# Kernel tuning notes

Hardware: AMD Instinct MI355X
Metric: run time of the kernel (lower is better)

## Reference

```python
import jax, jax.numpy as jnp
import numpy as np

C = 256
C8 = C // 8


def setup_inputs() -> dict:
    key = jax.random.key(0)
    ks = jax.random.split(key, 9)
    B, H, W = 4, 64, 64
    s = 1.0 / np.sqrt(C)
    return {
        "pre_feat": jax.random.normal(ks[0], (B, C, H, W), jnp.float32),
        "post_feat": jax.random.normal(ks[1], (B, C, H, W), jnp.float32),
        "Wq": jax.random.normal(ks[2], (C8, C), jnp.float32) * s,
        "bq": jnp.zeros((C8,), jnp.float32),
        "Wk": jax.random.normal(ks[3], (C8, C), jnp.float32) * s,
        "bk": jnp.zeros((C8,), jnp.float32),
        "Wv": jax.random.normal(ks[4], (C, C), jnp.float32) * s,
        "bv": jnp.zeros((C,), jnp.float32),
        "gamma": jnp.zeros((1,), jnp.float32),
    }


def reference(pre_feat, post_feat, Wq, bq, Wk, bk, Wv, bv, gamma):
    B, Cc, H, W = pre_feat.shape
    N = H * W
    pre = pre_feat.reshape(B, Cc, N)    # (B, C, N)
    post = post_feat.reshape(B, Cc, N)
    # 1x1 convs == per-pixel linear projections
    q = jnp.einsum('dc,bcn->bdn', Wq, post) + bq[None, :, None]  # (B, C8, N)
    k = jnp.einsum('dc,bcn->bdn', Wk, pre) + bk[None, :, None]   # (B, C8, N)
    v = jnp.einsum('dc,bcn->bdn', Wv, pre) + bv[None, :, None]   # (B, C, N)
    # energy[b,i,j] = <q[b,:,i], k[b,:,j]>  (unscaled)
    energy = jnp.einsum('bdi,bdj->bij', q, k)                    # (B, N, N)
    attention = jax.nn.softmax(energy, axis=-1)
    # out[b,c,i] = sum_j v[b,c,j] * attention[b,i,j]
    out = jnp.einsum('bcj,bij->bci', v, attention).reshape(B, Cc, H, W)
    return gamma[0] * out + post_feat
```

## Files before the change

### kernel.cpp

```cpp
#include <hip/hip_runtime.h>

#define Bn 4
#define Cn 256
#define Dn 32
#define Nn 4096

typedef __bf16 bf16x8 __attribute__((ext_vector_type(8)));
typedef short shortx4 __attribute__((ext_vector_type(4)));
typedef float f32x4 __attribute__((ext_vector_type(4)));

__device__ __forceinline__ float bf2f(unsigned short u) {
  unsigned int v = ((unsigned int)u) << 16;
  return __builtin_bit_cast(float, v);
}
__device__ __forceinline__ unsigned short f2bf(float f) {
  unsigned int v = __builtin_bit_cast(unsigned int, f);
  v += 0x7FFFu + ((v >> 16) & 1u);
  return (unsigned short)(v >> 16);
}
__device__ __forceinline__ bf16x8 ldfrag(const unsigned short* p) {
  return __builtin_bit_cast(bf16x8, *(const uint4*)p);
}
__device__ __forceinline__ uint4 pack8(const float* p) {
  float4 a = *(const float4*)p;
  float4 b = *(const float4*)(p + 4);
  union { unsigned short s[8]; uint4 u; } x;
  x.s[0] = f2bf(a.x); x.s[1] = f2bf(a.y); x.s[2] = f2bf(a.z); x.s[3] = f2bf(a.w);
  x.s[4] = f2bf(b.x); x.s[5] = f2bf(b.y); x.s[6] = f2bf(b.z); x.s[7] = f2bf(b.w);
  return x.u;
}
__device__ __forceinline__ uint4 pack4x2(const float* p0, const float* p1) {
  float4 a = *(const float4*)p0;
  float4 b = *(const float4*)p1;
  union { unsigned short s[8]; uint4 u; } x;
  x.s[0] = f2bf(a.x); x.s[1] = f2bf(a.y); x.s[2] = f2bf(a.z); x.s[3] = f2bf(a.w);
  x.s[4] = f2bf(b.x); x.s[5] = f2bf(b.y); x.s[6] = f2bf(b.z); x.s[7] = f2bf(b.w);
  return x.u;
}
__device__ __forceinline__ void async16(unsigned short* lds, const unsigned short* g) {
  __builtin_amdgcn_global_load_lds(
      (const __attribute__((address_space(1))) unsigned int*)g,
      (__attribute__((address_space(3))) unsigned int*)lds, 16, 0, 0);
}

__global__ __launch_bounds__(256) void conv_weights(
    const float* __restrict__ Wq, const float* __restrict__ Wk,
    const float* __restrict__ Wv, unsigned short* __restrict__ WqBf,
    unsigned short* __restrict__ WkBf, unsigned short* __restrict__ WvBf)
{
  int idx8 = (blockIdx.x * 256 + threadIdx.x) * 8;
  if (idx8 < 8192) {
    *(uint4*)(WqBf + idx8) = pack8(Wq + idx8);
  } else if (idx8 < 16384) {
    *(uint4*)(WkBf + idx8 - 8192) = pack8(Wk + idx8 - 8192);
  } else {
    *(uint4*)(WvBf + idx8 - 16384) = pack8(Wv + idx8 - 16384);
  }
}

__global__ __launch_bounds__(256) void qk_proj(
    const float* __restrict__ pre, const float* __restrict__ post,
    const unsigned short* __restrict__ WqBf, const float* __restrict__ bq,
    const unsigned short* __restrict__ WkBf, const float* __restrict__ bk,
    unsigned short* __restrict__ Qt, unsigned short* __restrict__ Kt,
    unsigned short* __restrict__ preBf)
{
  __shared__ __align__(16) unsigned short sPre[64][40];
  __shared__ __align__(16) unsigned short sPost[64][40];
  __shared__ __align__(16) float sRed[4][64][16];

  const int tid = threadIdx.x;
  const int lane = tid & 63, w = tid >> 6;
  const int quad = lane >> 4, n16 = lane & 15;
  const int b = blockIdx.x >> 7;
  const int i0 = (blockIdx.x & 127) << 5;
  const int iSub = w & 1, cHalf = w >> 1;

  const float* preB = pre + (size_t)b * Cn * Nn;
  const float* postB = post + (size_t)b * Cn * Nn;

  const f32x4 zz = {0.f, 0.f, 0.f, 0.f};
  f32x4 accQ[2] = {zz, zz}, accK[2] = {zz, zz};

  const int cc = tid >> 2, q = tid & 3;
  const int gcol = ((n16 >> 2) << 3) + (iSub << 2) + (n16 & 3);

  for (int it = 0; it < 4; it++) {
    const int cs = it * 64;
    const float* pPost = postB + (size_t)(cs + cc) * Nn + i0;
    const float* pPre  = preB  + (size_t)(cs + cc) * Nn + i0;
    uint4 pkPost = pack4x2(pPost + q * 4, pPost + 16 + q * 4);
    uint4 pkPre  = pack4x2(pPre  + q * 4, pPre  + 16 + q * 4);
    __syncthreads();
    *(uint4*)&sPost[cc][q * 8] = pkPost;
    *(uint4*)&sPre[cc][q * 8]  = pkPre;
    *(uint4*)(preBf + ((size_t)b * Cn + cs + cc) * Nn + i0 + q * 8) = pkPre;
    __syncthreads();

    union { unsigned short s[8]; bf16x8 v; } up, ur;
#pragma unroll
    for (int jj = 0; jj < 8; jj++) {
      up.s[jj] = sPost[cHalf * 32 + quad * 8 + jj][gcol];
      ur.s[jj] = sPre[cHalf * 32 + quad * 8 + jj][gcol];
    }
    const int c0g = cs + cHalf * 32 + quad * 8;
#pragma unroll
    for (int dt = 0; dt < 2; dt++) {
      bf16x8 aq = ldfrag(WqBf + (size_t)(dt * 16 + n16) * Cn + c0g);
      accQ[dt] = __builtin_amdgcn_mfma_f32_16x16x32_bf16(aq, up.v, accQ[dt], 0, 0, 0);
      bf16x8 ak = ldfrag(WkBf + (size_t)(dt * 16 + n16) * Cn + c0g);
      accK[dt] = __builtin_amdgcn_mfma_f32_16x16x32_bf16(ak, ur.v, accK[dt], 0, 0, 0);
    }
  }

  __syncthreads();
#pragma unroll
  for (int dt = 0; dt < 2; dt++) {
    *(f32x4*)&sRed[w][lane][dt * 4] = accQ[dt];
    *(f32x4*)&sRed[w][lane][8 + dt * 4] = accK[dt];
  }
  __syncthreads();
  if (w < 2) {
    const int ii = i0 + iSub * 16 + n16;
#pragma unroll
    for (int dt = 0; dt < 2; dt++) {
      f32x4 qv = *(f32x4*)&sRed[w][lane][dt * 4];
      f32x4 q2 = *(f32x4*)&sRed[w + 2][lane][dt * 4];
      f32x4 kv = *(f32x4*)&sRed[w][lane][8 + dt * 4];
      f32x4 k2 = *(f32x4*)&sRed[w + 2][lane][8 + dt * 4];
      union { unsigned short s[4]; uint2 u; } oq, ok;
#pragma unroll
      for (int r = 0; r < 4; r++) {
        int d = dt * 16 + quad * 4 + r;
        oq.s[r] = f2bf(qv[r] + q2[r] + bq[d]);
        ok.s[r] = f2bf(kv[r] + k2[r] + bk[d]);
      }
      *(uint2*)(Qt + ((size_t)b * Nn + ii) * Dn + dt * 16 + quad * 4) = oq.u;
      *(uint2*)(Kt + ((size_t)b * Nn + ii) * Dn + dt * 16 + quad * 4) = ok.u;
    }
  }
}

__global__ __launch_bounds__(128, 2) void flash_attn(
    const unsigned short* __restrict__ Qt, const unsigned short* __restrict__ Kt,
    const unsigned short* __restrict__ preBf,
    unsigned short* __restrict__ Opart, float* __restrict__ Lpart)
{
  __shared__ __align__(16) unsigned short sX[256 * 64];
  __shared__ __align__(16) unsigned short sK[64][40];

  const int tid = threadIdx.x;
  const int lane = tid & 63, w = tid >> 6;
  const int quad = lane >> 4, n16 = lane & 15;
  const int b = blockIdx.x >> 8;
  const int js = (blockIdx.x >> 6) & 3;
  const int it = blockIdx.x & 63;
  const int iw = it * 64 + w * 32;

  bf16x8 qf[2];
#pragma unroll
  for (int sub = 0; sub < 2; sub++)
    qf[sub] = ldfrag(Qt + ((size_t)b * Nn + iw + sub * 16 + n16) * Dn + quad * 8);

  const f32x4 zz = {0.f, 0.f, 0.f, 0.f};
  f32x4 acc[2][16];
#pragma unroll
  for (int sub = 0; sub < 2; sub++)
#pragma unroll
    for (int ct = 0; ct < 16; ct++) acc[sub][ct] = zz;
  float lrow[2] = {0.f, 0.f};

  const int lrw = lane >> 3;
  const size_t laneoff = (size_t)lrw * Nn + (size_t)(((lane & 7) ^ lrw) << 3);
  const unsigned short* preB = preBf + (size_t)b * Cn * Nn + laneoff;
  const int xsw = n16 & 7;
  const int xoff0 = ((quad) ^ xsw) << 3;
  const int xoff1 = ((4 + quad) ^ xsw) << 3;

  for (int j0 = js * 1024; j0 < js * 1024 + 1024; j0 += 64) {
    __syncthreads();
#pragma unroll
    for (int k = 0; k < 2; k++) {
      int s = tid + k * 128;
      int row = s >> 2, seg = (s & 3) << 3;
      *(uint4*)&sK[row][seg] =
          *(const uint4*)(Kt + ((size_t)b * Nn + j0 + row) * Dn + seg);
    }
#pragma unroll
    for (int k = 0; k < 16; k++) {
      const int rb = (k * 2 + w) * 8;
      async16(sX + rb * 64 + (lane << 3), preB + (size_t)rb * Nn + j0);
    }
    __syncthreads();

    f32x4 sc[2][4];
#pragma unroll
    for (int jt = 0; jt < 4; jt++) {
      bf16x8 akf = ldfrag(&sK[jt * 16 + n16][quad * 8]);
      sc[0][jt] = __builtin_amdgcn_mfma_f32_16x16x32_bf16(akf, qf[0], zz, 0, 0, 0);
      sc[1][jt] = __builtin_amdgcn_mfma_f32_16x16x32_bf16(akf, qf[1], zz, 0, 0, 0);
    }

    shortx4 pb[2][4];
#pragma unroll
    for (int sub = 0; sub < 2; sub++) {
      float ps = 0.f;
#pragma unroll
      for (int jt = 0; jt < 4; jt++) {
        union { unsigned short s[4]; shortx4 v; } u;
#pragma unroll
        for (int r = 0; r < 4; r++) {
          float p = __expf(fminf(sc[sub][jt][r], 70.f));
          ps += p;
          u.s[r] = f2bf(p);
        }
        pb[sub][jt] = u.v;
      }
      ps += __shfl_xor(ps, 16);
      ps += __shfl_xor(ps, 32);
      lrow[sub] += ps;
    }

#pragma unroll
    for (int jt2 = 0; jt2 < 2; jt2++) {
      const int xoff = jt2 ? xoff1 : xoff0;
#pragma unroll
      for (int ct = 0; ct < 16; ct++) {
        union { bf16x8 v; shortx4 h[2]; } av;
        av.v = ldfrag(&sX[(ct * 16 + n16) * 64 + xoff]);
        acc[0][ct] = __builtin_amdgcn_mfma_f32_16x16x16bf16_1k(av.h[0], pb[0][jt2 * 2], acc[0][ct], 0, 0, 0);
        acc[0][ct] = __builtin_amdgcn_mfma_f32_16x16x16bf16_1k(av.h[1], pb[0][jt2 * 2 + 1], acc[0][ct], 0, 0, 0);
        acc[1][ct] = __builtin_amdgcn_mfma_f32_16x16x16bf16_1k(av.h[0], pb[1][jt2 * 2], acc[1][ct], 0, 0, 0);
        acc[1][ct] = __builtin_amdgcn_mfma_f32_16x16x16bf16_1k(av.h[1], pb[1][jt2 * 2 + 1], acc[1][ct], 0, 0, 0);
      }
    }
  }

  const size_t base = (size_t)(js * 4 + b) * Nn;
#pragma unroll
  for (int sub = 0; sub < 2; sub++) {
    const int i = iw + sub * 16 + n16;
    if (quad == 0) Lpart[base + i] = lrow[sub];
#pragma unroll
    for (int ct = 0; ct < 16; ct++) {
      union { unsigned short s[4]; uint2 u; } pk;
#pragma unroll
      for (int r = 0; r < 4; r++) pk.s[r] = f2bf(acc[sub][ct][r]);
      *(uint2*)(Opart + (base + i) * 256 + ct * 16 + quad * 4) = pk.u;
    }
  }
}

__global__ __launch_bounds__(256) void combine(
    const unsigned short* __restrict__ Opart, const float* __restrict__ Lpart,
    const unsigned short* __restrict__ WvBf, const float* __restrict__ bv,
    const float* __restrict__ post, const float* __restrict__ gamma,
    float* __restrict__ out)
{
  __shared__ __align__(16) unsigned short sU[64 * 264];
  __shared__ float sL[64];

  const int tid = threadIdx.x;
  const int lane = tid & 63, w = tid >> 6;
  const int quad = lane >> 4, n16 = lane & 15;
  const int b = blockIdx.x >> 6;
  const int i0 = (blockIdx.x & 63) << 6;

  if (tid < 64) {
    float l = 0.f;
#pragma unroll
    for (int js = 0; js < 4; js++) l += Lpart[(size_t)(js * 4 + b) * Nn + i0 + tid];
    sL[tid] = 1.f / l;
  }
  __syncthreads();

#pragma unroll
  for (int pass = 0; pass < 8; pass++) {
    const int il = pass * 8 + (tid >> 5);
    const int c8 = (tid & 31) << 3;
    const float inv = sL[il];
    float a[8] = {0.f, 0.f, 0.f, 0.f, 0.f, 0.f, 0.f, 0.f};
#pragma unroll
    for (int js = 0; js < 4; js++) {
      uint4 u = *(const uint4*)(Opart + ((size_t)(js * 4 + b) * Nn + i0 + il) * 256 + c8);
      const unsigned short* us = (const unsigned short*)&u;
#pragma unroll
      for (int e = 0; e < 8; e++) a[e] += bf2f(us[e]);
    }
    union { unsigned short s[8]; uint4 u; } pk;
#pragma unroll
    for (int e = 0; e < 8; e++) pk.s[e] = f2bf(a[e] * inv);
    *(uint4*)&sU[il * 264 + c8] = pk.u;
  }
  __syncthreads();

  bf16x8 ub[8];
#pragma unroll
  for (int kc = 0; kc < 8; kc++)
    ub[kc] = ldfrag(&sU[(w * 16 + n16) * 264 + kc * 32 + quad * 8]);

  const float g = gamma[0];
  const f32x4 zz = {0.f, 0.f, 0.f, 0.f};
#pragma unroll
  for (int ct2 = 0; ct2 < 16; ct2++) {
    f32x4 o = zz;
#pragma unroll
    for (int kc = 0; kc < 8; kc++) {
      bf16x8 awv = ldfrag(WvBf + (size_t)(ct2 * 16 + n16) * Cn + kc * 32 + quad * 8);
      o = __builtin_amdgcn_mfma_f32_16x16x32_bf16(awv, ub[kc], o, 0, 0, 0);
    }
#pragma unroll
    for (int r = 0; r < 4; r++) {
      const int c = ct2 * 16 + quad * 4 + r;
      const size_t addr = ((size_t)b * Cn + c) * Nn + i0 + w * 16 + n16;
      out[addr] = g * (o[r] + bv[c]) + post[addr];
    }
  }
}

extern "C" void kernel_launch(void* const* d_in, const int* in_sizes, int n_in,
                              void* d_out, int out_size, void* d_ws, size_t ws_size,
                              hipStream_t stream) {
  const float* pre   = (const float*)d_in[0];
  const float* post  = (const float*)d_in[1];
  const float* Wq    = (const float*)d_in[2];
  const float* bq    = (const float*)d_in[3];
  const float* Wk    = (const float*)d_in[4];
  const float* bk    = (const float*)d_in[5];
  const float* Wv    = (const float*)d_in[6];
  const float* bv    = (const float*)d_in[7];
  const float* gamma = (const float*)d_in[8];
  float* out = (float*)d_out;

  char* ws = (char*)d_ws;
  unsigned short* Qt    = (unsigned short*)ws;
  unsigned short* Kt    = Qt + (size_t)Bn * Nn * Dn;
  unsigned short* preBf = Kt + (size_t)Bn * Nn * Dn;
  unsigned short* WqBf  = preBf + (size_t)Bn * Cn * Nn;
  unsigned short* WkBf  = WqBf + Dn * Cn;
  unsigned short* WvBf  = WkBf + Dn * Cn;
  unsigned short* Opart = WvBf + Cn * Cn;
  float* Lpart = (float*)(Opart + (size_t)4 * Bn * Nn * Cn);

  conv_weights<<<40, 256, 0, stream>>>(Wq, Wk, Wv, WqBf, WkBf, WvBf);
  qk_proj<<<512, 256, 0, stream>>>(pre, post, WqBf, bq, WkBf, bk, Qt, Kt, preBf);
  flash_attn<<<1024, 128, 0, stream>>>(Qt, Kt, preBf, Opart, Lpart);
  combine<<<256, 256, 0, stream>>>(Opart, Lpart, WvBf, bv, post, gamma, out);
}
```

Baseline: 215.8 us.

## Restructure prep/projection, pipeline flash attention K/P, and regrid combine

The weight conversion is merged with a new prep kernel that converts pre and post to bf16 and writes pixel-major transposed copies, so qk_proj becomes a plain MFMA loop over contiguous rows. Q is prescaled by log2(e) so the softmax uses exp2f. The flash attention loop now loads K fragments straight from global into registers and computes the next tile's probabilities while the current tile's PV MFMAs run, removing the K shared-memory staging. The combine kernel uses 512 smaller blocks, and packed bf16 conversion intrinsics replace manual rounding. The cost is an extra transposed bf16 copy of the inputs aliased into the Opart workspace, plus more registers in flash_attn.

```diff
diff --git a/kernel.cpp b/kernel.cpp
--- a/kernel.cpp
+++ b/kernel.cpp
@@ -1,4 +1,5 @@
 #include <hip/hip_runtime.h>
+#include <hip/hip_bf16.h>
 
 #define Bn 4
 #define Cn 256
@@ -18,23 +19,20 @@
   v += 0x7FFFu + ((v >> 16) & 1u);
   return (unsigned short)(v >> 16);
 }
+__device__ __forceinline__ unsigned int pk2(float a, float b) {
+  union { __hip_bfloat162 h; unsigned int u; } x;
+  x.h = __float22bfloat162_rn(make_float2(a, b));
+  return x.u;
+}
 __device__ __forceinline__ bf16x8 ldfrag(const unsigned short* p) {
   return __builtin_bit_cast(bf16x8, *(const uint4*)p);
 }
 __device__ __forceinline__ uint4 pack8(const float* p) {
   float4 a = *(const float4*)p;
   float4 b = *(const float4*)(p + 4);
-  union { unsigned short s[8]; uint4 u; } x;
-  x.s[0] = f2bf(a.x); x.s[1] = f2bf(a.y); x.s[2] = f2bf(a.z); x.s[3] = f2bf(a.w);
-  x.s[4] = f2bf(b.x); x.s[5] = f2bf(b.y); x.s[6] = f2bf(b.z); x.s[7] = f2bf(b.w);
-  return x.u;
-}
-__device__ __forceinline__ uint4 pack4x2(const float* p0, const float* p1) {
-  float4 a = *(const float4*)p0;
-  float4 b = *(const float4*)p1;
-  union { unsigned short s[8]; uint4 u; } x;
-  x.s[0] = f2bf(a.x); x.s[1] = f2bf(a.y); x.s[2] = f2bf(a.z); x.s[3] = f2bf(a.w);
-  x.s[4] = f2bf(b.x); x.s[5] = f2bf(b.y); x.s[6] = f2bf(b.z); x.s[7] = f2bf(b.w);
+  union { unsigned int u2[4]; uint4 u; } x;
+  x.u2[0] = pk2(a.x, a.y); x.u2[1] = pk2(a.z, a.w);
+  x.u2[2] = pk2(b.x, b.y); x.u2[3] = pk2(b.z, b.w);
   return x.u;
 }
 __device__ __forceinline__ void async16(unsigned short* lds, const unsigned short* g) {
@@ -43,102 +41,100 @@
       (__attribute__((address_space(3))) unsigned int*)lds, 16, 0, 0);
 }
 
-__global__ __launch_bounds__(256) void conv_weights(
+__global__ __launch_bounds__(256) void prep(
+    const float* __restrict__ pre, const float* __restrict__ post,
     const float* __restrict__ Wq, const float* __restrict__ Wk,
-    const float* __restrict__ Wv, unsigned short* __restrict__ WqBf,
+    const float* __restrict__ Wv,
+    unsigned short* __restrict__ preT, unsigned short* __restrict__ postT,
+    unsigned short* __restrict__ preBf, unsigned short* __restrict__ WqBf,
     unsigned short* __restrict__ WkBf, unsigned short* __restrict__ WvBf)
 {
-  int idx8 = (blockIdx.x * 256 + threadIdx.x) * 8;
-  if (idx8 < 8192) {
-    *(uint4*)(WqBf + idx8) = pack8(Wq + idx8);
-  } else if (idx8 < 16384) {
-    *(uint4*)(WkBf + idx8 - 8192) = pack8(Wk + idx8 - 8192);
-  } else {
-    *(uint4*)(WvBf + idx8 - 16384) = pack8(Wv + idx8 - 16384);
-  }
+  if (blockIdx.x >= 1024) {
+    int idx8 = ((blockIdx.x - 1024) * 256 + threadIdx.x) * 8;
+    if (idx8 < 8192) {
+      *(uint4*)(WqBf + idx8) = pack8(Wq + idx8);
+    } else if (idx8 < 16384) {
+      *(uint4*)(WkBf + idx8 - 8192) = pack8(Wk + idx8 - 8192);
+    } else {
+      *(uint4*)(WvBf + idx8 - 16384) = pack8(Wv + idx8 - 16384);
+    }
+    return;
+  }
+  __shared__ __align__(16) unsigned short sA[64][72];
+  __shared__ __align__(16) unsigned short sB[64][72];
+  const int tid = threadIdx.x;
+  const int b = blockIdx.x >> 8;
+  const int c0 = ((blockIdx.x >> 6) & 3) << 6;
+  const int i0 = (blockIdx.x & 63) << 6;
+  const int r = tid >> 2, ch = (tid & 3) << 4;
+
+  const float* pPost = post + ((size_t)b * Cn + c0 + r) * Nn + i0 + ch;
+  const float* pPre  = pre  + ((size_t)b * Cn + c0 + r) * Nn + i0 + ch;
+  *(uint4*)&sA[r][ch]     = pack8(pPost);
+  *(uint4*)&sA[r][ch + 8] = pack8(pPost + 8);
+  uint4 pb0 = pack8(pPre), pb1 = pack8(pPre + 8);
+  *(uint4*)&sB[r][ch]     = pb0;
+  *(uint4*)&sB[r][ch + 8] = pb1;
+  __syncthreads();
+
+#pragma unroll
+  for (int e = 0; e < 2; e++) {
+    int h = ((tid & 3) << 1) + e;
+    int g = (h >> 2) << 5, q = (h & 3) << 2;
+    union { unsigned short s[8]; uint4 u; } o;
+    *(uint2*)&o.s[0] = *(const uint2*)&sB[r][g + q];
+    *(uint2*)&o.s[4] = *(const uint2*)&sB[r][g + 16 + q];
+    *(uint4*)(preBf + ((size_t)b * Cn + c0 + r) * Nn + i0 + h * 8) = o.u;
+  }
+  union { unsigned short s[16]; uint4 u[2]; } tp, tk;
+#pragma unroll
+  for (int e = 0; e < 16; e++) {
+    tp.s[e] = sA[ch + e][r];
+    tk.s[e] = sB[ch + e][r];
+  }
+  const size_t trow = ((size_t)b * Nn + i0 + r) * Cn + c0 + ch;
+  *(uint4*)(postT + trow) = tp.u[0];
+  *(uint4*)(postT + trow + 8) = tp.u[1];
+  *(uint4*)(preT + trow) = tk.u[0];
+  *(uint4*)(preT + trow + 8) = tk.u[1];
 }
 
 __global__ __launch_bounds__(256) void qk_proj(
-    const float* __restrict__ pre, const float* __restrict__ post,
+    const unsigned short* __restrict__ preT, const unsigned short* __restrict__ postT,
     const unsigned short* __restrict__ WqBf, const float* __restrict__ bq,
     const unsigned short* __restrict__ WkBf, const float* __restrict__ bk,
-    unsigned short* __restrict__ Qt, unsigned short* __restrict__ Kt,
-    unsigned short* __restrict__ preBf)
+    unsigned short* __restrict__ Qt, unsigned short* __restrict__ Kt)
 {
-  __shared__ __align__(16) unsigned short sPre[64][40];
-  __shared__ __align__(16) unsigned short sPost[64][40];
-  __shared__ __align__(16) float sRed[4][64][16];
-
   const int tid = threadIdx.x;
   const int lane = tid & 63, w = tid >> 6;
   const int quad = lane >> 4, n16 = lane & 15;
   const int b = blockIdx.x >> 7;
   const int i0 = (blockIdx.x & 127) << 5;
-  const int iSub = w & 1, cHalf = w >> 1;
-
-  const float* preB = pre + (size_t)b * Cn * Nn;
-  const float* postB = post + (size_t)b * Cn * Nn;
+  const int isub = w & 1, dh = w >> 1;
+  const int i = i0 + isub * 16 + n16;
+  const size_t rowB = ((size_t)b * Nn + i) * Cn;
 
   const f32x4 zz = {0.f, 0.f, 0.f, 0.f};
-  f32x4 accQ[2] = {zz, zz}, accK[2] = {zz, zz};
-
-  const int cc = tid >> 2, q = tid & 3;
-  const int gcol = ((n16 >> 2) << 3) + (iSub << 2) + (n16 & 3);
-
-  for (int it = 0; it < 4; it++) {
-    const int cs = it * 64;
-    const float* pPost = postB + (size_t)(cs + cc) * Nn + i0;
-    const float* pPre  = preB  + (size_t)(cs + cc) * Nn + i0;
-    uint4 pkPost = pack4x2(pPost + q * 4, pPost + 16 + q * 4);
-    uint4 pkPre  = pack4x2(pPre  + q * 4, pPre  + 16 + q * 4);
-    __syncthreads();
-    *(uint4*)&sPost[cc][q * 8] = pkPost;
-    *(uint4*)&sPre[cc][q * 8]  = pkPre;
-    *(uint4*)(preBf + ((size_t)b * Cn + cs + cc) * Nn + i0 + q * 8) = pkPre;
-    __syncthreads();
-
-    union { unsigned short s[8]; bf16x8 v; } up, ur;
-#pragma unroll
-    for (int jj = 0; jj < 8; jj++) {
-      up.s[jj] = sPost[cHalf * 32 + quad * 8 + jj][gcol];
-      ur.s[jj] = sPre[cHalf * 32 + quad * 8 + jj][gcol];
-    }
-    const int c0g = cs + cHalf * 32 + quad * 8;
-#pragma unroll
-    for (int dt = 0; dt < 2; dt++) {
-      bf16x8 aq = ldfrag(WqBf + (size_t)(dt * 16 + n16) * Cn + c0g);
-      accQ[dt] = __builtin_amdgcn_mfma_f32_16x16x32_bf16(aq, up.v, accQ[dt], 0, 0, 0);
-      bf16x8 ak = ldfrag(WkBf + (size_t)(dt * 16 + n16) * Cn + c0g);
-      accK[dt] = __builtin_amdgcn_mfma_f32_16x16x32_bf16(ak, ur.v, accK[dt], 0, 0, 0);
-    }
-  }
-
-  __syncthreads();
-#pragma unroll
-  for (int dt = 0; dt < 2; dt++) {
-    *(f32x4*)&sRed[w][lane][dt * 4] = accQ[dt];
-    *(f32x4*)&sRed[w][lane][8 + dt * 4] = accK[dt];
-  }
-  __syncthreads();
-  if (w < 2) {
-    const int ii = i0 + iSub * 16 + n16;
-#pragma unroll
-    for (int dt = 0; dt < 2; dt++) {
-      f32x4 qv = *(f32x4*)&sRed[w][lane][dt * 4];
-      f32x4 q2 = *(f32x4*)&sRed[w + 2][lane][dt * 4];
-      f32x4 kv = *(f32x4*)&sRed[w][lane][8 + dt * 4];
-      f32x4 k2 = *(f32x4*)&sRed[w + 2][lane][8 + dt * 4];
-      union { unsigned short s[4]; uint2 u; } oq, ok;
-#pragma unroll
-      for (int r = 0; r < 4; r++) {
-        int d = dt * 16 + quad * 4 + r;
-        oq.s[r] = f2bf(qv[r] + q2[r] + bq[d]);
-        ok.s[r] = f2bf(kv[r] + k2[r] + bk[d]);
-      }
-      *(uint2*)(Qt + ((size_t)b * Nn + ii) * Dn + dt * 16 + quad * 4) = oq.u;
-      *(uint2*)(Kt + ((size_t)b * Nn + ii) * Dn + dt * 16 + quad * 4) = ok.u;
-    }
-  }
+  f32x4 aq = zz, ak = zz;
+#pragma unroll
+  for (int kc = 0; kc < 8; kc++) {
+    bf16x8 bfq = ldfrag(postT + rowB + kc * 32 + quad * 8);
+    bf16x8 bfk = ldfrag(preT + rowB + kc * 32 + quad * 8);
+    bf16x8 awq = ldfrag(WqBf + (size_t)(dh * 16 + n16) * Cn + kc * 32 + quad * 8);
+    bf16x8 awk = ldfrag(WkBf + (size_t)(dh * 16 + n16) * Cn + kc * 32 + quad * 8);
+    aq = __builtin_amdgcn_mfma_f32_16x16x32_bf16(awq, bfq, aq, 0, 0, 0);
+    ak = __builtin_amdgcn_mfma_f32_16x16x32_bf16(awk, bfk, ak, 0, 0, 0);
+  }
+  const float LOG2E = 1.44269504f;
+  union { unsigned short s[4]; uint2 u; } oq, ok;
+#pragma unroll
+  for (int r = 0; r < 4; r++) {
+    int d = dh * 16 + quad * 4 + r;
+    oq.s[r] = f2bf((aq[r] + bq[d]) * LOG2E);
+    ok.s[r] = f2bf(ak[r] + bk[d]);
+  }
+  *(uint2*)(Qt + ((size_t)b * Nn + i) * Dn + dh * 16 + quad * 4) = oq.u;
+  *(uint2*)(Kt + ((size_t)b * Nn + i) * Dn + dh * 16 + quad * 4) = ok.u;
 }
 
 __global__ __launch_bounds__(128, 2) void flash_attn(
@@ -147,7 +143,6 @@
     unsigned short* __restrict__ Opart, float* __restrict__ Lpart)
 {
   __shared__ __align__(16) unsigned short sX[256 * 64];
-  __shared__ __align__(16) unsigned short sK[64][40];
 
   const int tid = threadIdx.x;
   const int lane = tid & 63, w = tid >> 6;
@@ -156,6 +151,7 @@
   const int js = (blockIdx.x >> 6) & 3;
   const int it = blockIdx.x & 63;
   const int iw = it * 64 + w * 32;
+  const int jbase = js * 1024;
 
   bf16x8 qf[2];
 #pragma unroll
@@ -174,52 +170,62 @@
   const size_t laneoff = (size_t)lrw * Nn + (size_t)(((lane & 7) ^ lrw) << 3);
   const unsigned short* preB = preBf + (size_t)b * Cn * Nn + laneoff;
   const int xsw = n16 & 7;
-  const int xoff0 = ((quad) ^ xsw) << 3;
+  const int xoff0 = (quad ^ xsw) << 3;
   const int xoff1 = ((4 + quad) ^ xsw) << 3;
 
-  for (int j0 = js * 1024; j0 < js * 1024 + 1024; j0 += 64) {
-    __syncthreads();
-#pragma unroll
-    for (int k = 0; k < 2; k++) {
-      int s = tid + k * 128;
-      int row = s >> 2, seg = (s & 3) << 3;
-      *(uint4*)&sK[row][seg] =
-          *(const uint4*)(Kt + ((size_t)b * Nn + j0 + row) * Dn + seg);
-    }
+  auto stage = [&](int j0) {
 #pragma unroll
     for (int k = 0; k < 16; k++) {
       const int rb = (k * 2 + w) * 8;
       async16(sX + rb * 64 + (lane << 3), preB + (size_t)rb * Nn + j0);
     }
-    __syncthreads();
-
+  };
+  auto loadK = [&](int j0, bf16x8 kf[4]) {
+#pragma unroll
+    for (int jt = 0; jt < 4; jt++)
+      kf[jt] = ldfrag(Kt + ((size_t)b * Nn + j0 + jt * 16 + n16) * Dn + quad * 8);
+  };
+  auto makeP = [&](const bf16x8 kf[4], shortx4 pbDst[2][4]) {
     f32x4 sc[2][4];
 #pragma unroll
     for (int jt = 0; jt < 4; jt++) {
-      bf16x8 akf = ldfrag(&sK[jt * 16 + n16][quad * 8]);
-      sc[0][jt] = __builtin_amdgcn_mfma_f32_16x16x32_bf16(akf, qf[0], zz, 0, 0, 0);
-      sc[1][jt] = __builtin_amdgcn_mfma_f32_16x16x32_bf16(akf, qf[1], zz, 0, 0, 0);
-    }
-
-    shortx4 pb[2][4];
+      sc[0][jt] = __builtin_amdgcn_mfma_f32_16x16x32_bf16(kf[jt], qf[0], zz, 0, 0, 0);
+      sc[1][jt] = __builtin_amdgcn_mfma_f32_16x16x32_bf16(kf[jt], qf[1], zz, 0, 0, 0);
+    }
 #pragma unroll
     for (int sub = 0; sub < 2; sub++) {
       float ps = 0.f;
 #pragma unroll
       for (int jt = 0; jt < 4; jt++) {
-        union { unsigned short s[4]; shortx4 v; } u;
-#pragma unroll
-        for (int r = 0; r < 4; r++) {
-          float p = __expf(fminf(sc[sub][jt][r], 70.f));
-          ps += p;
-          u.s[r] = f2bf(p);
-        }
-        pb[sub][jt] = u.v;
+        float p0 = exp2f(fminf(sc[sub][jt][0], 101.f));
+        float p1 = exp2f(fminf(sc[sub][jt][1], 101.f));
+        float p2 = exp2f(fminf(sc[sub][jt][2], 101.f));
+        float p3 = exp2f(fminf(sc[sub][jt][3], 101.f));
+        ps += (p0 + p1) + (p2 + p3);
+        union { unsigned int u2[2]; shortx4 v; } u;
+        u.u2[0] = pk2(p0, p1);
+        u.u2[1] = pk2(p2, p3);
+        pbDst[sub][jt] = u.v;
       }
       ps += __shfl_xor(ps, 16);
       ps += __shfl_xor(ps, 32);
       lrow[sub] += ps;
     }
+  };
+
+  stage(jbase);
+  shortx4 pb[2][4];
+  {
+    bf16x8 kf0[4];
+    loadK(jbase, kf0);
+    makeP(kf0, pb);
+  }
+  __syncthreads();
+
+  for (int t = 0; t < 16; ++t) {
+    const int jn = jbase + (t + 1) * 64;
+    bf16x8 kfn[4];
+    if (t < 15) loadK(jn, kfn);
 
 #pragma unroll
     for (int jt2 = 0; jt2 < 2; jt2++) {
@@ -234,6 +240,17 @@
         acc[1][ct] = __builtin_amdgcn_mfma_f32_16x16x16bf16_1k(av.h[1], pb[1][jt2 * 2 + 1], acc[1][ct], 0, 0, 0);
       }
     }
+    __syncthreads();
+    if (t < 15) {
+      stage(jn);
+      shortx4 pbn[2][4];
+      makeP(kfn, pbn);
+#pragma unroll
+      for (int sub = 0; sub < 2; sub++)
+#pragma unroll
+        for (int jt = 0; jt < 4; jt++) pb[sub][jt] = pbn[sub][jt];
+    }
+    __syncthreads();
   }
 
   const size_t base = (size_t)(js * 4 + b) * Nn;
@@ -243,9 +260,9 @@
     if (quad == 0) Lpart[base + i] = lrow[sub];
 #pragma unroll
     for (int ct = 0; ct < 16; ct++) {
-      union { unsigned short s[4]; uint2 u; } pk;
-#pragma unroll
-      for (int r = 0; r < 4; r++) pk.s[r] = f2bf(acc[sub][ct][r]);
+      union { unsigned int u2[2]; uint2 u; } pk;
+      pk.u2[0] = pk2(acc[sub][ct][0], acc[sub][ct][1]);
+      pk.u2[1] = pk2(acc[sub][ct][2], acc[sub][ct][3]);
       *(uint2*)(Opart + (base + i) * 256 + ct * 16 + quad * 4) = pk.u;
     }
   }
@@ -257,16 +274,16 @@
     const float* __restrict__ post, const float* __restrict__ gamma,
     float* __restrict__ out)
 {
-  __shared__ __align__(16) unsigned short sU[64 * 264];
-  __shared__ float sL[64];
+  __shared__ __align__(16) unsigned short sU[32 * 264];
+  __shared__ float sL[32];
 
   const int tid = threadIdx.x;
   const int lane = tid & 63, w = tid >> 6;
   const int quad = lane >> 4, n16 = lane & 15;
-  const int b = blockIdx.x >> 6;
-  const int i0 = (blockIdx.x & 63) << 6;
-
-  if (tid < 64) {
+  const int b = blockIdx.x >> 7;
+  const int i0 = (blockIdx.x & 127) << 5;
+
+  if (tid < 32) {
     float l = 0.f;
 #pragma unroll
     for (int js = 0; js < 4; js++) l += Lpart[(size_t)(js * 4 + b) * Nn + i0 + tid];
@@ -274,46 +291,52 @@
   }
   __syncthreads();
 
-#pragma unroll
-  for (int pass = 0; pass < 8; pass++) {
-    const int il = pass * 8 + (tid >> 5);
-    const int c8 = (tid & 31) << 3;
-    const float inv = sL[il];
+  const int il = tid >> 3, cbase = (tid & 7) << 5;
+  const float inv = sL[il];
+#pragma unroll
+  for (int u4 = 0; u4 < 4; u4++) {
+    const int c8 = cbase + u4 * 8;
     float a[8] = {0.f, 0.f, 0.f, 0.f, 0.f, 0.f, 0.f, 0.f};
 #pragma unroll
     for (int js = 0; js < 4; js++) {
-      uint4 u = *(const uint4*)(Opart + ((size_t)(js * 4 + b) * Nn + i0 + il) * 256 + c8);
-      const unsigned short* us = (const unsigned short*)&u;
+      uint4 uu = *(const uint4*)(Opart + ((size_t)(js * 4 + b) * Nn + i0 + il) * 256 + c8);
+      const unsigned short* us = (const unsigned short*)&uu;
 #pragma unroll
       for (int e = 0; e < 8; e++) a[e] += bf2f(us[e]);
     }
-    union { unsigned short s[8]; uint4 u; } pk;
-#pragma unroll
-    for (int e = 0; e < 8; e++) pk.s[e] = f2bf(a[e] * inv);
+    union { unsigned int u2[4]; uint4 u; } pk;
+#pragma unroll
+    for (int e2 = 0; e2 < 4; e2++) pk.u2[e2] = pk2(a[2 * e2] * inv, a[2 * e2 + 1] * inv);
     *(uint4*)&sU[il * 264 + c8] = pk.u;
   }
   __syncthreads();
 
-  bf16x8 ub[8];
-#pragma unroll
-  for (int kc = 0; kc < 8; kc++)
-    ub[kc] = ldfrag(&sU[(w * 16 + n16) * 264 + kc * 32 + quad * 8]);
+  bf16x8 ub[2][8];
+#pragma unroll
+  for (int sub = 0; sub < 2; sub++)
+#pragma unroll
+    for (int kc = 0; kc < 8; kc++)
+      ub[sub][kc] = ldfrag(&sU[(sub * 16 + n16) * 264 + kc * 32 + quad * 8]);
 
   const float g = gamma[0];
   const f32x4 zz = {0.f, 0.f, 0.f, 0.f};
 #pragma unroll
-  for (int ct2 = 0; ct2 < 16; ct2++) {
-    f32x4 o = zz;
+  for (int e = 0; e < 4; e++) {
+    const int ct2 = w * 4 + e;
+    f32x4 o0 = zz, o1 = zz;
 #pragma unroll
     for (int kc = 0; kc < 8; kc++) {
       bf16x8 awv = ldfrag(WvBf + (size_t)(ct2 * 16 + n16) * Cn + kc * 32 + quad * 8);
-      o = __builtin_amdgcn_mfma_f32_16x16x32_bf16(awv, ub[kc], o, 0, 0, 0);
+      o0 = __builtin_amdgcn_mfma_f32_16x16x32_bf16(awv, ub[0][kc], o0, 0, 0, 0);
+      o1 = __builtin_amdgcn_mfma_f32_16x16x32_bf16(awv, ub[1][kc], o1, 0, 0, 0);
     }
 #pragma unroll
     for (int r = 0; r < 4; r++) {
       const int c = ct2 * 16 + quad * 4 + r;
-      const size_t addr = ((size_t)b * Cn + c) * Nn + i0 + w * 16 + n16;
-      out[addr] = g * (o[r] + bv[c]) + post[addr];
+      const float bb = bv[c];
+      size_t a0 = ((size_t)b * Cn + c) * Nn + i0 + n16;
+      out[a0] = g * (o0[r] + bb) + post[a0];
+      out[a0 + 16] = g * (o1[r] + bb) + post[a0 + 16];
     }
   }
 }
@@ -332,18 +355,21 @@
   const float* gamma = (const float*)d_in[8];
   float* out = (float*)d_out;
 
-  char* ws = (char*)d_ws;
-  unsigned short* Qt    = (unsigned short*)ws;
+  unsigned short* ws = (unsigned short*)d_ws;
+  unsigned short* Qt    = ws;
   unsigned short* Kt    = Qt + (size_t)Bn * Nn * Dn;
   unsigned short* preBf = Kt + (size_t)Bn * Nn * Dn;
   unsigned short* WqBf  = preBf + (size_t)Bn * Cn * Nn;
   unsigned short* WkBf  = WqBf + Dn * Cn;
   unsigned short* WvBf  = WkBf + Dn * Cn;
-  unsigned short* Opart = WvBf + Cn * Cn;
-  float* Lpart = (float*)(Opart + (size_t)4 * Bn * Nn * Cn);
-
-  conv_weights<<<40, 256, 0, stream>>>(Wq, Wk, Wv, WqBf, WkBf, WvBf);
-  qk_proj<<<512, 256, 0, stream>>>(pre, post, WqBf, bq, WkBf, bk, Qt, Kt, preBf);
+  float* Lpart = (float*)(WvBf + Cn * Cn);
+  unsigned short* Opart = (unsigned short*)(Lpart + 4 * Bn * Nn);
+  unsigned short* preT  = Opart;
+  unsigned short* postT = Opart + (size_t)Bn * Nn * Cn;
+
+  prep<<<1064, 256, 0, stream>>>(pre, post, Wq, Wk, Wv,
+                                 preT, postT, preBf, WqBf, WkBf, WvBf);
+  qk_proj<<<512, 256, 0, stream>>>(preT, postT, WqBf, bq, WkBf, bk, Qt, Kt);
   flash_attn<<<1024, 128, 0, stream>>>(Qt, Kt, preBf, Opart, Lpart);
-  combine<<<256, 256, 0, stream>>>(Opart, Lpart, WvBf, bv, post, gamma, out);
-}
+  combine<<<512, 256, 0, stream>>>(Opart, Lpart, WvBf, bv, post, gamma, out);
+}
```

Result: faster. 202.7 us (-6.1%).
